# Kernel optimization log

Measured on AMD Instinct MI355X. Metric: run time of the kernel, lower is better.

## Reference

```python
import jax, jax.numpy as jnp
import numpy as np

D_MODEL = 1024
NUM_HEADS = 16
HEAD_DIM = D_MODEL // NUM_HEADS
B, S, L_CACHE = 2, 1024, 1024


def setup_inputs() -> dict:
    key = jax.random.key(0)
    ks = jax.random.split(key, 12)
    sc = 1.0 / np.sqrt(D_MODEL)
    return {
        "x": jax.random.normal(ks[0], (B, S, D_MODEL), jnp.float32),
        "cache_k": jax.random.normal(ks[1], (B, NUM_HEADS, L_CACHE, HEAD_DIM), jnp.float32),
        "cache_v": jax.random.normal(ks[2], (B, NUM_HEADS, L_CACHE, HEAD_DIM), jnp.float32),
        "Wq": jax.random.normal(ks[3], (D_MODEL, D_MODEL), jnp.float32) * sc,
        "bq": jax.random.normal(ks[4], (D_MODEL,), jnp.float32) * 0.01,
        "Wk": jax.random.normal(ks[5], (D_MODEL, D_MODEL), jnp.float32) * sc,
        "bk": jax.random.normal(ks[6], (D_MODEL,), jnp.float32) * 0.01,
        "Wv": jax.random.normal(ks[7], (D_MODEL, D_MODEL), jnp.float32) * sc,
        "bv": jax.random.normal(ks[8], (D_MODEL,), jnp.float32) * 0.01,
        "Wo": jax.random.normal(ks[9], (D_MODEL, D_MODEL), jnp.float32) * sc,
        "bo": jax.random.normal(ks[10], (D_MODEL,), jnp.float32) * 0.01,
    }


def reference(x, cache_k, cache_v, Wq, bq, Wk, bk, Wv, bv, Wo, bo):
    b, s, d = x.shape
    h, hd = NUM_HEADS, HEAD_DIM
    # torch Linear: y = x @ W^T + b
    def proj(W, bias):
        y = jnp.einsum('bsd,ed->bse', x, W) + bias
        return y.reshape(b, s, h, hd).transpose(0, 2, 1, 3)  # [B,H,S,hd]
    Q = proj(Wq, bq)
    K = jnp.concatenate([cache_k, proj(Wk, bk)], axis=2)  # [B,H,T,hd]
    V = jnp.concatenate([cache_v, proj(Wv, bv)], axis=2)
    T = K.shape[2]
    scores = jnp.einsum('bhqd,bhkd->bhqk', Q, K) / jnp.sqrt(jnp.float32(hd))
    # causal mask with cache offset: query i sees keys j <= i + (T - s)
    offset = T - s
    q_idx = jnp.arange(s)[:, None]
    k_idx = jnp.arange(T)[None, :]
    mask = k_idx > (q_idx + offset)  # [S,T], True = masked
    scores = jnp.where(mask[None, None], -jnp.inf, scores)
    attn = jax.nn.softmax(scores, axis=-1)
    out = jnp.einsum('bhqk,bhkd->bhqd', attn, V)
    out = out.transpose(0, 2, 1, 3).reshape(b, s, d)
    return jnp.einsum('bsd,ed->bse', out, Wo) + bo
```

## Files before the change

kernel.cpp:

```cpp
#include <hip/hip_runtime.h>
#include <hip/hip_bf16.h>
#include <stdint.h>

typedef __bf16 bf16;
typedef __bf16 bf16x4 __attribute__((ext_vector_type(4)));
typedef __bf16 bf16x8 __attribute__((ext_vector_type(8)));
typedef float  f32x4  __attribute__((ext_vector_type(4)));

#define DEV __device__ __forceinline__

#define BB 2
#define HH 16
#define SS 1024
#define DD 1024
#define HD 64
#define LC 1024
#define TT 2048
#define OFFS 1024

DEV f32x4 mfma16(bf16x8 a, bf16x8 b, f32x4 c) {
    return __builtin_amdgcn_mfma_f32_16x16x32_bf16(a, b, c, 0, 0, 0);
}

DEV void async_load16(const bf16* g, bf16* lds) {
    auto gp = reinterpret_cast<const __attribute__((address_space(1))) void*>(
        reinterpret_cast<uintptr_t>(g));
    auto lp = reinterpret_cast<__attribute__((address_space(3))) void*>(
        reinterpret_cast<uintptr_t>(lds));
    __builtin_amdgcn_global_load_lds(gp, lp, 16, 0, 0);
}

__global__ __launch_bounds__(256) void cvt_all(
    const float* __restrict__ x,  bf16* __restrict__ xb,
    const float* __restrict__ w0, const float* __restrict__ w1,
    const float* __restrict__ w2, const float* __restrict__ w3,
    bf16* __restrict__ d0, bf16* __restrict__ d1,
    bf16* __restrict__ d2, bf16* __restrict__ d3,
    const float* __restrict__ ck, bf16* __restrict__ Kf,
    const float* __restrict__ cv, bf16* __restrict__ Vt) {
    __shared__ float tile[64][65];
    const int bid = blockIdx.x;
    const int tid = threadIdx.x;
    if (bid < 8192) {
        const float* s;
        bf16* d;
        int i;
        if (bid < 2048) {
            s = x; d = xb; i = bid * 256 + tid;
        } else if (bid < 6144) {
            int which = (bid - 2048) >> 10;
            s = which == 0 ? w0 : which == 1 ? w1 : which == 2 ? w2 : w3;
            d = which == 0 ? d0 : which == 1 ? d1 : which == 2 ? d2 : d3;
            i = ((bid - 2048) & 1023) * 256 + tid;
        } else {
            int ii = (bid - 6144) * 256 + tid;
            int bh  = ii >> 14;
            int rem = ii & 16383;
            s = ck; d = Kf + (size_t)bh * TT * HD - (size_t)bh * LC * HD;
            i = ii;
            float4 v = ((const float4*)s)[i];
            bf16x4 o;
            o[0] = (bf16)v.x; o[1] = (bf16)v.y; o[2] = (bf16)v.z; o[3] = (bf16)v.w;
            ((bf16x4*)(Kf + (size_t)bh * TT * HD))[rem] = o;
            return;
        }
        float4 v = ((const float4*)s)[i];
        bf16x4 o;
        o[0] = (bf16)v.x; o[1] = (bf16)v.y; o[2] = (bf16)v.z; o[3] = (bf16)v.w;
        ((bf16x4*)d)[i] = o;
    } else {
        int rem = bid - 8192;
        int bh = rem >> 4;
        int t0 = (rem & 15) * 64;
        int c4 = (tid & 15) * 4;
        int rr = tid >> 4;
        const float* src = cv + ((size_t)bh * LC + t0) * HD;
#pragma unroll
        for (int p = 0; p < 4; ++p) {
            int t = rr + p * 16;
            float4 v = *(const float4*)(src + (size_t)t * HD + c4);
            tile[c4 + 0][t] = v.x; tile[c4 + 1][t] = v.y;
            tile[c4 + 2][t] = v.z; tile[c4 + 3][t] = v.w;
        }
        __syncthreads();
        bf16* dst = Vt + (size_t)bh * HD * TT + t0;
#pragma unroll
        for (int p = 0; p < 4; ++p) {
            int d = rr + p * 16;
            int tc = (tid & 15) * 4;
            bf16x4 o;
            o[0] = (bf16)tile[d][tc + 0]; o[1] = (bf16)tile[d][tc + 1];
            o[2] = (bf16)tile[d][tc + 2]; o[3] = (bf16)tile[d][tc + 3];
            *(bf16x4*)(dst + (size_t)d * TT + tc) = o;
        }
    }
}

__global__ __launch_bounds__(256) void gemm_nt(
    const bf16* __restrict__ Xb, const bf16* __restrict__ Ob,
    const bf16* __restrict__ Wqb, const bf16* __restrict__ Wkb,
    const bf16* __restrict__ Wvb, const bf16* __restrict__ Wob,
    const float* __restrict__ bq, const float* __restrict__ bk,
    const float* __restrict__ bv, const float* __restrict__ bo,
    bf16* __restrict__ Qb, bf16* __restrict__ Kf, bf16* __restrict__ Vt,
    float* __restrict__ Out, int mode_base) {
    const int mode = mode_base + blockIdx.z;
    const bf16* A  = (mode == 3) ? Ob : Xb;
    const bf16* Wp = (mode == 0) ? Wqb : (mode == 1) ? Wkb : (mode == 2) ? Wvb : Wob;
    const float* bias = (mode == 0) ? bq : (mode == 1) ? bk : (mode == 2) ? bv : bo;

    const int tid  = threadIdx.x;
    const int wv   = tid >> 6;
    const int lane = tid & 63;
    const int l16  = lane & 15;
    const int quad = lane >> 4;
    const int wm = (wv >> 1) * 64;
    const int wn = (wv & 1) * 64;
    const int m0 = blockIdx.y * 128;
    const int n0 = blockIdx.x * 128;

    __shared__ __align__(16) bf16 As[128 * 64];
    __shared__ __align__(16) bf16 Bs[128 * 64];

    f32x4 acc[4][4];
#pragma unroll
    for (int i = 0; i < 4; ++i)
#pragma unroll
        for (int j = 0; j < 4; ++j) {
            f32x4 z = {0.f, 0.f, 0.f, 0.f};
            acc[i][j] = z;
        }

    const int r8 = lane >> 3;
    const int s8 = lane & 7;
    const int arow = wv * 32;

    for (int k0 = 0; k0 < 1024; k0 += 64) {
#pragma unroll
        for (int c = 0; c < 4; ++c) {
            int row = arow + c * 8 + r8;
            async_load16(A  + (size_t)(m0 + row) * 1024 + k0 + s8 * 8, As + row * 64 + s8 * 8);
            async_load16(Wp + (size_t)(n0 + row) * 1024 + k0 + s8 * 8, Bs + row * 64 + s8 * 8);
        }
        __syncthreads();
#pragma unroll
        for (int kk = 0; kk < 64; kk += 32) {
            bf16x8 af[4], bfr[4];
#pragma unroll
            for (int i = 0; i < 4; ++i)
                af[i] = *(const bf16x8*)(As + (wm + i * 16 + l16) * 64 + kk + quad * 8);
#pragma unroll
            for (int j = 0; j < 4; ++j)
                bfr[j] = *(const bf16x8*)(Bs + (wn + j * 16 + l16) * 64 + kk + quad * 8);
#pragma unroll
            for (int i = 0; i < 4; ++i)
#pragma unroll
                for (int j = 0; j < 4; ++j)
                    acc[i][j] = mfma16(af[i], bfr[j], acc[i][j]);
        }
        __syncthreads();
    }

#pragma unroll
    for (int i = 0; i < 4; ++i) {
#pragma unroll
        for (int j = 0; j < 4; ++j) {
            int n = n0 + wn + j * 16 + l16;
            float bval = bias[n];
#pragma unroll
            for (int r = 0; r < 4; ++r) {
                int m = m0 + wm + i * 16 + quad * 4 + r;
                float v = acc[i][j][r] + bval;
                if (mode == 3) {
                    Out[(size_t)m * 1024 + n] = v;
                } else {
                    int b = m >> 10, s = m & 1023;
                    int h = n >> 6,  d = n & 63;
                    int bh = b * HH + h;
                    if (mode == 0)
                        Qb[((size_t)bh * SS + s) * HD + d] = (bf16)v;
                    else if (mode == 1)
                        Kf[((size_t)bh * TT + LC + s) * HD + d] = (bf16)v;
                    else
                        Vt[((size_t)bh * HD + d) * TT + LC + s] = (bf16)v;
                }
            }
        }
    }
}

__global__ __launch_bounds__(256) void attn(const bf16* __restrict__ Qb,
                                            const bf16* __restrict__ Kf,
                                            const bf16* __restrict__ Vt,
                                            bf16* __restrict__ Ob) {
    const int i = blockIdx.x;
    const int bh = i & 31;
    const int qblk = (i < 256) ? (15 - (i >> 5)) : ((i >> 5) - 8);
    const int tid  = threadIdx.x;
    const int wv   = tid >> 6;
    const int lane = tid & 63;
    const int l16  = lane & 15;
    const int quad = lane >> 4;
    const int qb   = qblk * 64;
    const int qw   = qb + wv * 16;

    const bf16* Qp = Qb + ((size_t)bh * SS + qw) * HD;
    const bf16* Kp = Kf + (size_t)bh * TT * HD;
    const bf16* Vp = Vt + (size_t)bh * HD * TT;

    __shared__ __align__(16) bf16 Ks[2][64 * 64];
    __shared__ __align__(16) bf16 Vs[2][64 * 64];

    bf16x8 qf0 = *(const bf16x8*)(Qp + l16 * HD + quad * 8);
    bf16x8 qf1 = *(const bf16x8*)(Qp + l16 * HD + 32 + quad * 8);

    float lsum = 0.f;
    f32x4 o[4];
#pragma unroll
    for (int dt = 0; dt < 4; ++dt) {
        f32x4 z = {0.f, 0.f, 0.f, 0.f};
        o[dt] = z;
    }

    const int niters = qblk + 17;

    auto stage = [&](int tile, int b) {
        const int t0 = tile * 64;
#pragma unroll
        for (int j = 0; j < 2; ++j) {
            int seg = (j * 4 + wv) * 64 + lane;
            int row = seg >> 3;
            int gc  = (seg & 7) ^ (row & 7);
            async_load16(Kp + (size_t)(t0 + row) * HD + gc * 8, &Ks[b][seg * 8]);
            async_load16(Vp + (size_t)row * TT + t0 + gc * 8, &Vs[b][seg * 8]);
        }
    };

    stage(0, 0);

    const float C1 = 0.18033688f;
    const float C2 = -11.5415603f;

    for (int it = 0; it < niters; ++it) {
        __syncthreads();
        const bf16* Kb = &Ks[it & 1][0];
        const bf16* Vb = &Vs[it & 1][0];
        if (it + 1 < niters) stage(it + 1, (it + 1) & 1);

        const int t0 = it * 64;
        const bool full = (t0 + 63 <= qw + OFFS);

        f32x4 s[4];
#pragma unroll
        for (int kt = 0; kt < 4; ++kt) {
            int row = kt * 16 + l16;
            int swz = row & 7;
            bf16x8 ka = *(const bf16x8*)(Kb + (row * 8 + (quad ^ swz)) * 8);
            bf16x8 kb = *(const bf16x8*)(Kb + (row * 8 + ((4 + quad) ^ swz)) * 8);
            f32x4 z = {0.f, 0.f, 0.f, 0.f};
            z = mfma16(ka, qf0, z);
            z = mfma16(kb, qf1, z);
            s[kt] = z;
        }

        f32x4 p[4];
        if (full) {
#pragma unroll
            for (int kt = 0; kt < 4; ++kt)
#pragma unroll
                for (int r = 0; r < 4; ++r)
                    p[kt][r] = __builtin_amdgcn_exp2f(fmaf(s[kt][r], C1, C2));
        } else {
            const int qlim = qw + l16 + OFFS - t0;
#pragma unroll
            for (int kt = 0; kt < 4; ++kt)
#pragma unroll
                for (int r = 0; r < 4; ++r) {
                    int tl = kt * 16 + quad * 4 + r;
                    float e = __builtin_amdgcn_exp2f(fmaf(s[kt][r], C1, C2));
                    p[kt][r] = (tl <= qlim) ? e : 0.f;
                }
        }
#pragma unroll
        for (int kt = 0; kt < 4; ++kt)
            lsum += (p[kt][0] + p[kt][1]) + (p[kt][2] + p[kt][3]);

        bf16x8 pf0, pf1;
#pragma unroll
        for (int j = 0; j < 4; ++j) {
            pf0[j]     = (bf16)p[0][j];
            pf0[4 + j] = (bf16)p[1][j];
            pf1[j]     = (bf16)p[2][j];
            pf1[4 + j] = (bf16)p[3][j];
        }

        const int q1 = quad >> 1;
        const int h4 = (quad & 1) * 4;
#pragma unroll
        for (int dt = 0; dt < 4; ++dt) {
            int row = dt * 16 + l16;
            int swz = row & 7;
            bf16x4 v0 = *(const bf16x4*)(Vb + (row * 8 + ((0 + q1) ^ swz)) * 8 + h4);
            bf16x4 v1 = *(const bf16x4*)(Vb + (row * 8 + ((2 + q1) ^ swz)) * 8 + h4);
            bf16x4 v2 = *(const bf16x4*)(Vb + (row * 8 + ((4 + q1) ^ swz)) * 8 + h4);
            bf16x4 v3 = *(const bf16x4*)(Vb + (row * 8 + ((6 + q1) ^ swz)) * 8 + h4);
            bf16x8 vf0, vf1;
#pragma unroll
            for (int j = 0; j < 4; ++j) {
                vf0[j] = v0[j]; vf0[4 + j] = v1[j];
                vf1[j] = v2[j]; vf1[4 + j] = v3[j];
            }
            o[dt] = mfma16(vf0, pf0, o[dt]);
            o[dt] = mfma16(vf1, pf1, o[dt]);
        }
    }

    lsum += __shfl_xor(lsum, 16, 64);
    lsum += __shfl_xor(lsum, 32, 64);
    const float rl = 1.f / lsum;

    const int b = bh >> 4, h = bh & 15;
    const int q = qw + l16;
    bf16* op = Ob + (((size_t)(b * SS + q) * HH) + h) * HD;
#pragma unroll
    for (int dt = 0; dt < 4; ++dt) {
        bf16x4 w;
#pragma unroll
        for (int r = 0; r < 4; ++r) w[r] = (bf16)(o[dt][r] * rl);
        *(bf16x4*)(op + dt * 16 + quad * 4) = w;
    }
}

extern "C" void kernel_launch(void* const* d_in, const int* in_sizes, int n_in,
                              void* d_out, int out_size, void* d_ws, size_t ws_size,
                              hipStream_t stream) {
    const float* x   = (const float*)d_in[0];
    const float* ck  = (const float*)d_in[1];
    const float* cv  = (const float*)d_in[2];
    const float* Wq  = (const float*)d_in[3];
    const float* bq  = (const float*)d_in[4];
    const float* Wk  = (const float*)d_in[5];
    const float* bk  = (const float*)d_in[6];
    const float* Wv  = (const float*)d_in[7];
    const float* bv  = (const float*)d_in[8];
    const float* Wo  = (const float*)d_in[9];
    const float* bo  = (const float*)d_in[10];
    float* out = (float*)d_out;

    char* ws = (char*)d_ws;
    bf16* xb  = (bf16*)(ws);
    bf16* wqb = (bf16*)(ws + ( 4u << 20));
    bf16* wkb = (bf16*)(ws + ( 6u << 20));
    bf16* wvb = (bf16*)(ws + ( 8u << 20));
    bf16* wob = (bf16*)(ws + (10u << 20));
    bf16* Qb  = (bf16*)(ws + (12u << 20));
    bf16* Kf  = (bf16*)(ws + (16u << 20));
    bf16* Vt  = (bf16*)(ws + (24u << 20));
    bf16* Ob  = (bf16*)(ws + (32u << 20));

    cvt_all<<<8704, 256, 0, stream>>>(x, xb, Wq, Wk, Wv, Wo, wqb, wkb, wvb, wob,
                                      ck, Kf, cv, Vt);

    gemm_nt<<<dim3(8, 16, 3), 256, 0, stream>>>(xb, Ob, wqb, wkb, wvb, wob,
                                                bq, bk, bv, bo, Qb, Kf, Vt, out, 0);
    attn<<<512, 256, 0, stream>>>(Qb, Kf, Vt, Ob);
    gemm_nt<<<dim3(8, 16, 1), 256, 0, stream>>>(xb, Ob, wqb, wkb, wvb, wob,
                                                bq, bk, bv, bo, Qb, Kf, Vt, out, 3);
}
```

Baseline: 186.0 us.

## Double-buffer GEMM LDS tiles with XOR swizzle and smaller M tiles

The projection GEMM now double-buffers its LDS tiles, so the next K slice loads asynchronously while MFMAs run on the current one. That needs only one barrier per iteration instead of two. LDS rows use an XOR swizzle to avoid bank conflicts. The M tile shrinks from 128 to 64 rows, and the QKV launch treats the contiguous Wq/Wk/Wv bf16 buffers as one 3072-row weight, which raises the block count for better CU coverage. The QKV launch depends on the workspace layout keeping those three weights adjacent, and each block now re-reads more A data.

```diff
diff --git a/kernel.cpp b/kernel.cpp
--- a/kernel.cpp
+++ b/kernel.cpp
@@ -56,9 +56,7 @@
             int ii = (bid - 6144) * 256 + tid;
             int bh  = ii >> 14;
             int rem = ii & 16383;
-            s = ck; d = Kf + (size_t)bh * TT * HD - (size_t)bh * LC * HD;
-            i = ii;
-            float4 v = ((const float4*)s)[i];
+            float4 v = ((const float4*)ck)[ii];
             bf16x4 o;
             o[0] = (bf16)v.x; o[1] = (bf16)v.y; o[2] = (bf16)v.z; o[3] = (bf16)v.w;
             ((bf16x4*)(Kf + (size_t)bh * TT * HD))[rem] = o;
@@ -97,85 +95,96 @@
 }
 
 __global__ __launch_bounds__(256) void gemm_nt(
-    const bf16* __restrict__ Xb, const bf16* __restrict__ Ob,
-    const bf16* __restrict__ Wqb, const bf16* __restrict__ Wkb,
-    const bf16* __restrict__ Wvb, const bf16* __restrict__ Wob,
+    const bf16* __restrict__ A, const bf16* __restrict__ W,
     const float* __restrict__ bq, const float* __restrict__ bk,
     const float* __restrict__ bv, const float* __restrict__ bo,
     bf16* __restrict__ Qb, bf16* __restrict__ Kf, bf16* __restrict__ Vt,
-    float* __restrict__ Out, int mode_base) {
-    const int mode = mode_base + blockIdx.z;
-    const bf16* A  = (mode == 3) ? Ob : Xb;
-    const bf16* Wp = (mode == 0) ? Wqb : (mode == 1) ? Wkb : (mode == 2) ? Wvb : Wob;
-    const float* bias = (mode == 0) ? bq : (mode == 1) ? bk : (mode == 2) ? bv : bo;
-
+    float* __restrict__ Out, int is_oproj) {
     const int tid  = threadIdx.x;
     const int wv   = tid >> 6;
     const int lane = tid & 63;
     const int l16  = lane & 15;
     const int quad = lane >> 4;
-    const int wm = (wv >> 1) * 64;
-    const int wn = (wv & 1) * 64;
-    const int m0 = blockIdx.y * 128;
+    const int m0 = blockIdx.y * 64;
     const int n0 = blockIdx.x * 128;
-
-    __shared__ __align__(16) bf16 As[128 * 64];
-    __shared__ __align__(16) bf16 Bs[128 * 64];
-
-    f32x4 acc[4][4];
+    const int mode = is_oproj ? 3 : (n0 >> 10);
+    const float* bias = (mode == 0) ? bq : (mode == 1) ? bk : (mode == 2) ? bv : bo;
+
+    __shared__ __align__(16) bf16 As[2][64 * 64];
+    __shared__ __align__(16) bf16 Bs[2][128 * 64];
+
+    f32x4 acc[4][2];
 #pragma unroll
     for (int i = 0; i < 4; ++i)
 #pragma unroll
-        for (int j = 0; j < 4; ++j) {
+        for (int j = 0; j < 2; ++j) {
             f32x4 z = {0.f, 0.f, 0.f, 0.f};
             acc[i][j] = z;
         }
 
-    const int r8 = lane >> 3;
-    const int s8 = lane & 7;
-    const int arow = wv * 32;
-
-    for (int k0 = 0; k0 < 1024; k0 += 64) {
-#pragma unroll
-        for (int c = 0; c < 4; ++c) {
-            int row = arow + c * 8 + r8;
-            async_load16(A  + (size_t)(m0 + row) * 1024 + k0 + s8 * 8, As + row * 64 + s8 * 8);
-            async_load16(Wp + (size_t)(n0 + row) * 1024 + k0 + s8 * 8, Bs + row * 64 + s8 * 8);
-        }
+    auto stage = [&](int k0, int b) {
+#pragma unroll
+        for (int k = 0; k < 2; ++k) {
+            int seg = k * 256 + tid;
+            int row = seg >> 3;
+            int c   = (seg & 7) ^ (row & 7);
+            async_load16(A + (size_t)(m0 + row) * 1024 + k0 + c * 8, &As[b][seg * 8]);
+        }
+#pragma unroll
+        for (int k = 0; k < 4; ++k) {
+            int seg = k * 256 + tid;
+            int row = seg >> 3;
+            int c   = (seg & 7) ^ (row & 7);
+            async_load16(W + (size_t)(n0 + row) * 1024 + k0 + c * 8, &Bs[b][seg * 8]);
+        }
+    };
+
+    stage(0, 0);
+
+    for (int it = 0; it < 16; ++it) {
         __syncthreads();
-#pragma unroll
-        for (int kk = 0; kk < 64; kk += 32) {
-            bf16x8 af[4], bfr[4];
+        const bf16* Ab = &As[it & 1][0];
+        const bf16* Bb = &Bs[it & 1][0];
+        if (it + 1 < 16) stage((it + 1) * 64, (it + 1) & 1);
+
+#pragma unroll
+        for (int kk = 0; kk < 2; ++kk) {
+            bf16x8 af[4], bfr[2];
+#pragma unroll
+            for (int i = 0; i < 4; ++i) {
+                int row = i * 16 + l16;
+                int slot = (kk * 4 + quad) ^ (row & 7);
+                af[i] = *(const bf16x8*)(Ab + (row * 8 + slot) * 8);
+            }
+#pragma unroll
+            for (int j = 0; j < 2; ++j) {
+                int row = wv * 32 + j * 16 + l16;
+                int slot = (kk * 4 + quad) ^ (row & 7);
+                bfr[j] = *(const bf16x8*)(Bb + (row * 8 + slot) * 8);
+            }
 #pragma unroll
             for (int i = 0; i < 4; ++i)
-                af[i] = *(const bf16x8*)(As + (wm + i * 16 + l16) * 64 + kk + quad * 8);
-#pragma unroll
-            for (int j = 0; j < 4; ++j)
-                bfr[j] = *(const bf16x8*)(Bs + (wn + j * 16 + l16) * 64 + kk + quad * 8);
-#pragma unroll
-            for (int i = 0; i < 4; ++i)
-#pragma unroll
-                for (int j = 0; j < 4; ++j)
+#pragma unroll
+                for (int j = 0; j < 2; ++j)
                     acc[i][j] = mfma16(af[i], bfr[j], acc[i][j]);
         }
-        __syncthreads();
     }
 
 #pragma unroll
     for (int i = 0; i < 4; ++i) {
 #pragma unroll
-        for (int j = 0; j < 4; ++j) {
-            int n = n0 + wn + j * 16 + l16;
-            float bval = bias[n];
+        for (int j = 0; j < 2; ++j) {
+            int n = n0 + wv * 32 + j * 16 + l16;
+            float bval = bias[n & 1023];
 #pragma unroll
             for (int r = 0; r < 4; ++r) {
-                int m = m0 + wm + i * 16 + quad * 4 + r;
+                int m = m0 + i * 16 + quad * 4 + r;
                 float v = acc[i][j][r] + bval;
                 if (mode == 3) {
                     Out[(size_t)m * 1024 + n] = v;
                 } else {
                     int b = m >> 10, s = m & 1023;
-                    int h = n >> 6,  d = n & 63;
+                    int h = (n & 1023) >> 6, d = n & 63;
                     int bh = b * HH + h;
                     if (mode == 0)
                         Qb[((size_t)bh * SS + s) * HD + d] = (bf16)v;
@@ -361,9 +370,9 @@
     cvt_all<<<8704, 256, 0, stream>>>(x, xb, Wq, Wk, Wv, Wo, wqb, wkb, wvb, wob,
                                       ck, Kf, cv, Vt);
 
-    gemm_nt<<<dim3(8, 16, 3), 256, 0, stream>>>(xb, Ob, wqb, wkb, wvb, wob,
-                                                bq, bk, bv, bo, Qb, Kf, Vt, out, 0);
+    gemm_nt<<<dim3(24, 32), 256, 0, stream>>>(xb, wqb, bq, bk, bv, bo,
+                                              Qb, Kf, Vt, out, 0);
     attn<<<512, 256, 0, stream>>>(Qb, Kf, Vt, Ob);
-    gemm_nt<<<dim3(8, 16, 1), 256, 0, stream>>>(xb, Ob, wqb, wkb, wvb, wob,
-                                                bq, bk, bv, bo, Qb, Kf, Vt, out, 3);
-}
+    gemm_nt<<<dim3(8, 32), 256, 0, stream>>>(Ob, wob, bq, bk, bv, bo,
+                                             Qb, Kf, Vt, out, 1);
+}
```

Measured after the change: 160.3 us. -13.8%, faster.
